# Kernel tuning notes

Hardware: AMD Instinct MI355X
Metric: run time of the kernel (lower is better)

## Reference

```python
import jax, jax.numpy as jnp
import numpy as np

N_CLUSTERS = 8
ENC_IN = 862
SEQ_LEN = 720
PRED_LEN = 336
BATCH = 64


def setup_inputs() -> dict:
    key = jax.random.key(0)
    k1, k2, k3, k4 = jax.random.split(key, 4)
    x = jax.random.normal(k1, (BATCH, ENC_IN, SEQ_LEN), dtype=jnp.float32)
    clusters = jax.random.randint(k2, (ENC_IN,), 0, N_CLUSTERS, dtype=jnp.int64)
    # Per-cluster Linear(seq_len -> pred_len): weight [P, S], bias [P], like nn.Linear
    bound = 1.0 / np.sqrt(SEQ_LEN)
    W = jax.random.uniform(k3, (N_CLUSTERS, PRED_LEN, SEQ_LEN), dtype=jnp.float32, minval=-bound, maxval=bound)
    b = jax.random.uniform(k4, (N_CLUSTERS, PRED_LEN), dtype=jnp.float32, minval=-bound, maxval=bound)
    return {"x": x, "clusters": clusters, "W": W, "b": b}


def reference(x, clusters, W, b):
    # Gather each channel's cluster weight/bias, then batched per-channel GEMV.
    Wc = W[clusters]            # [C, P, S]
    bc = b[clusters]            # [C, P]
    # out[b, c, p] = sum_s x[b, c, s] * Wc[c, p, s] + bc[c, p]
    out = jnp.einsum('bcs,cps->bcp', x, Wc) + bc[None, :, :]
    return out
```

## Files before the change

kernel.cpp:

```cpp
#include <hip/hip_runtime.h>
#include <stdint.h>

#define N_CL    8
#define C_IN    862
#define SEQ     720
#define SEQP    768
#define PRED    336
#define BATCH   64
#define BK      64
#define NCH     (SEQP / BK)
#define XBSTRIDE ((size_t)C_IN * SEQ)

typedef __attribute__((ext_vector_type(8))) __bf16 bf16x8;
typedef __attribute__((ext_vector_type(4))) float  floatx4;

__device__ __forceinline__ void async16(const void* g, void* l) {
  __builtin_amdgcn_global_load_lds(
      (__attribute__((address_space(1))) unsigned int*)(uintptr_t)g,
      (__attribute__((address_space(3))) unsigned int*)l,
      16, 0, 0);
}

__global__ void wconv_kernel(const float* __restrict__ W, __bf16* __restrict__ Wb) {
  const int row = blockIdx.x;
  const float* src = W + (size_t)row * SEQ;
  __bf16* dst = Wb + (size_t)row * SEQP;
  for (int s = threadIdx.x; s < SEQP; s += blockDim.x) {
    float v = (s < SEQ) ? src[s] : 0.0f;
    dst[s] = (__bf16)v;
  }
}

#define A_BYTES 8192
#define B_BYTES 43008

__global__ __launch_bounds__(256, 3) void clin_kernel(
    const float* __restrict__ x, const int* __restrict__ clusters,
    const __bf16* __restrict__ Wb, const float* __restrict__ bias,
    float* __restrict__ out) {
  __shared__ __attribute__((aligned(128))) unsigned char smem[A_BYTES + B_BYTES];
  unsigned char* As = smem;
  unsigned char* Bs = smem + A_BYTES;

  const int c    = blockIdx.x;
  const int cl   = clusters[c];
  const int tid  = threadIdx.x;
  const int wave = tid >> 6;
  const int lane = tid & 63;
  const int q    = lane >> 4;
  const int ln   = lane & 15;
  const int m7   = ln & 7;

  const float*  xc = x  + (size_t)c * SEQ;
  const __bf16* wc = Wb + (size_t)cl * PRED * SEQP;

  floatx4 acc[4][5];
  floatx4 accx[4];
#pragma unroll
  for (int mt = 0; mt < 4; ++mt) {
#pragma unroll
    for (int t = 0; t < 5; ++t) acc[mt][t] = (floatx4){0.f, 0.f, 0.f, 0.f};
    accx[mt] = (floatx4){0.f, 0.f, 0.f, 0.f};
  }

  const int ar  = tid >> 2;
  const int ag0 = (tid & 3) << 1;
  const int am  = ar & 7;
  const uint32_t aoff0 = (uint32_t)ar * 128 + (((ag0    ) ^ am) << 4);
  const uint32_t aoff1 = (uint32_t)ar * 128 + (((ag0 + 1) ^ am) << 4);
  const float* asrc = xc + (size_t)ar * XBSTRIDE;

  const int bB_r  = lane >> 3;
  const int bB_pg = lane & 7;

  const int nb = wave * 5;

  for (int chunk = 0; chunk < NCH; ++chunk) {
    const int k0 = chunk * BK;

    for (int i = wave; i < 42; i += 4) {
      int r  = (i << 3) + bB_r;
      int lg = bB_pg ^ (r & 7);
      async16(wc + (size_t)r * SEQP + k0 + (lg << 3), Bs + i * 1024);
    }

    if (k0 + BK <= SEQ) {
      const float* s = asrc + k0 + (ag0 << 3);
      floatx4 f0 = *(const floatx4*)(s);
      floatx4 f1 = *(const floatx4*)(s + 4);
      floatx4 f2 = *(const floatx4*)(s + 8);
      floatx4 f3 = *(const floatx4*)(s + 12);
      bf16x8 h0, h1;
      h0[0] = (__bf16)f0[0]; h0[1] = (__bf16)f0[1];
      h0[2] = (__bf16)f0[2]; h0[3] = (__bf16)f0[3];
      h0[4] = (__bf16)f1[0]; h0[5] = (__bf16)f1[1];
      h0[6] = (__bf16)f1[2]; h0[7] = (__bf16)f1[3];
      h1[0] = (__bf16)f2[0]; h1[1] = (__bf16)f2[1];
      h1[2] = (__bf16)f2[2]; h1[3] = (__bf16)f2[3];
      h1[4] = (__bf16)f3[0]; h1[5] = (__bf16)f3[1];
      h1[6] = (__bf16)f3[2]; h1[7] = (__bf16)f3[3];
      *(bf16x8*)(As + aoff0) = h0;
      *(bf16x8*)(As + aoff1) = h1;
    } else {
      float tmp[16];
#pragma unroll
      for (int j = 0; j < 16; ++j) {
        int k = k0 + (ag0 << 3) + j;
        tmp[j] = (k < SEQ) ? asrc[k] : 0.0f;
      }
      bf16x8 h0, h1;
#pragma unroll
      for (int j = 0; j < 8; ++j) { h0[j] = (__bf16)tmp[j]; h1[j] = (__bf16)tmp[8 + j]; }
      *(bf16x8*)(As + aoff0) = h0;
      *(bf16x8*)(As + aoff1) = h1;
    }
    __syncthreads();

#pragma unroll
    for (int kk = 0; kk < BK; kk += 32) {
      const int gA = (kk >> 3) + q;
      bf16x8 a[4];
#pragma unroll
      for (int mt = 0; mt < 4; ++mt)
        a[mt] = *(const bf16x8*)(As + ((mt << 4) + ln) * 128 + ((gA ^ m7) << 4));
#pragma unroll
      for (int t = 0; t < 5; ++t) {
        int n = ((nb + t) << 4) + ln;
        bf16x8 b = *(const bf16x8*)(Bs + n * 128 + ((gA ^ m7) << 4));
#pragma unroll
        for (int mt = 0; mt < 4; ++mt)
          acc[mt][t] = __builtin_amdgcn_mfma_f32_16x16x32_bf16(a[mt], b, acc[mt][t], 0, 0, 0);
      }
      if (wave == 3) {
        int n = (20 << 4) + ln;
        bf16x8 b = *(const bf16x8*)(Bs + n * 128 + ((gA ^ m7) << 4));
#pragma unroll
        for (int mt = 0; mt < 4; ++mt)
          accx[mt] = __builtin_amdgcn_mfma_f32_16x16x32_bf16(a[mt], b, accx[mt], 0, 0, 0);
      }
    }
    __syncthreads();
  }

  const float* bc = bias + cl * PRED;
#pragma unroll
  for (int t = 0; t < 5; ++t) {
    int p = ((nb + t) << 4) + ln;
    float bv = bc[p];
#pragma unroll
    for (int mt = 0; mt < 4; ++mt) {
#pragma unroll
      for (int r = 0; r < 4; ++r) {
        int brow = (mt << 4) + (q << 2) + r;
        out[((size_t)brow * C_IN + c) * PRED + p] = acc[mt][t][r] + bv;
      }
    }
  }
  if (wave == 3) {
    int p = (20 << 4) + ln;
    float bv = bc[p];
#pragma unroll
    for (int mt = 0; mt < 4; ++mt) {
#pragma unroll
      for (int r = 0; r < 4; ++r) {
        int brow = (mt << 4) + (q << 2) + r;
        out[((size_t)brow * C_IN + c) * PRED + p] = accx[mt][r] + bv;
      }
    }
  }
}

extern "C" void kernel_launch(void* const* d_in, const int* in_sizes, int n_in,
                              void* d_out, int out_size, void* d_ws, size_t ws_size,
                              hipStream_t stream) {
  const float* x   = (const float*)d_in[0];
  const int*   cls = (const int*)d_in[1];
  const float* W   = (const float*)d_in[2];
  const float* b   = (const float*)d_in[3];
  float* out = (float*)d_out;
  __bf16* Wb = (__bf16*)d_ws;

  hipLaunchKernelGGL(wconv_kernel, dim3(N_CL * PRED), dim3(256), 0, stream, W, Wb);
  hipLaunchKernelGGL(clin_kernel, dim3(C_IN), dim3(256), 0, stream,
                     x, cls, Wb, b, out);
}
```

Before: 307.8 us.

## Split channel GEMV across two blocks and double-buffer LDS chunks

Each channel is now handled by two blocks, each taking half of the prediction rows (176 and 160), which doubles the grid and balances tiles across waves. The K loop is double-buffered: the next chunk's weight async loads and x global loads are issued before the MFMA work on the current chunk, and there is one barrier per iteration instead of two. This aims to overlap memory latency with compute and to spread work over more CUs. In exchange each block uses more LDS and occupancy is lowered to 2 blocks per CU, and each x tile is now read and converted twice.

```diff
diff --git a/kernel.cpp b/kernel.cpp
--- a/kernel.cpp
+++ b/kernel.cpp
@@ -6,10 +6,15 @@
 #define SEQ     720
 #define SEQP    768
 #define PRED    336
-#define BATCH   64
 #define BK      64
-#define NCH     (SEQP / BK)
+#define NCH     12
 #define XBSTRIDE ((size_t)C_IN * SEQ)
+
+#define H0_ROWS 176
+#define H1_ROWS 160
+#define A_BYTES 8192
+#define B_BYTES (H0_ROWS * 128)
+#define BUF_BYTES (A_BYTES + B_BYTES)
 
 typedef __attribute__((ext_vector_type(8))) __bf16 bf16x8;
 typedef __attribute__((ext_vector_type(4))) float  floatx4;
@@ -31,18 +36,19 @@
   }
 }
 
-#define A_BYTES 8192
-#define B_BYTES 43008
-
-__global__ __launch_bounds__(256, 3) void clin_kernel(
+__global__ __launch_bounds__(256, 2) void clin_kernel(
     const float* __restrict__ x, const int* __restrict__ clusters,
     const __bf16* __restrict__ Wb, const float* __restrict__ bias,
     float* __restrict__ out) {
-  __shared__ __attribute__((aligned(128))) unsigned char smem[A_BYTES + B_BYTES];
-  unsigned char* As = smem;
-  unsigned char* Bs = smem + A_BYTES;
-
-  const int c    = blockIdx.x;
+  __shared__ __attribute__((aligned(128))) unsigned char smem[2 * BUF_BYTES];
+
+  const int bid  = blockIdx.x;
+  const int c    = bid >> 1;
+  const int half = bid & 1;
+  const int nrows = half ? H1_ROWS : H0_ROWS;
+  const int ntl   = half ? 10 : 11;
+  const int prow0 = half * H0_ROWS;
+
   const int cl   = clusters[c];
   const int tid  = threadIdx.x;
   const int wave = tid >> 6;
@@ -52,16 +58,13 @@
   const int m7   = ln & 7;
 
   const float*  xc = x  + (size_t)c * SEQ;
-  const __bf16* wc = Wb + (size_t)cl * PRED * SEQP;
-
-  floatx4 acc[4][5];
-  floatx4 accx[4];
-#pragma unroll
-  for (int mt = 0; mt < 4; ++mt) {
-#pragma unroll
-    for (int t = 0; t < 5; ++t) acc[mt][t] = (floatx4){0.f, 0.f, 0.f, 0.f};
-    accx[mt] = (floatx4){0.f, 0.f, 0.f, 0.f};
-  }
+  const __bf16* wc = Wb + (size_t)cl * PRED * SEQP + (size_t)prow0 * SEQP;
+
+  floatx4 acc[4][3];
+#pragma unroll
+  for (int mt = 0; mt < 4; ++mt)
+#pragma unroll
+    for (int t = 0; t < 3; ++t) acc[mt][t] = (floatx4){0.f, 0.f, 0.f, 0.f};
 
   const int ar  = tid >> 2;
   const int ag0 = (tid & 3) << 1;
@@ -72,49 +75,67 @@
 
   const int bB_r  = lane >> 3;
   const int bB_pg = lane & 7;
-
-  const int nb = wave * 5;
-
-  for (int chunk = 0; chunk < NCH; ++chunk) {
-    const int k0 = chunk * BK;
-
-    for (int i = wave; i < 42; i += 4) {
+  const int nBi   = nrows >> 3;
+
+  {
+    unsigned char* As = smem;
+    unsigned char* Bs = smem + A_BYTES;
+    for (int i = wave; i < nBi; i += 4) {
       int r  = (i << 3) + bB_r;
       int lg = bB_pg ^ (r & 7);
-      async16(wc + (size_t)r * SEQP + k0 + (lg << 3), Bs + i * 1024);
-    }
-
-    if (k0 + BK <= SEQ) {
-      const float* s = asrc + k0 + (ag0 << 3);
-      floatx4 f0 = *(const floatx4*)(s);
-      floatx4 f1 = *(const floatx4*)(s + 4);
-      floatx4 f2 = *(const floatx4*)(s + 8);
-      floatx4 f3 = *(const floatx4*)(s + 12);
-      bf16x8 h0, h1;
-      h0[0] = (__bf16)f0[0]; h0[1] = (__bf16)f0[1];
-      h0[2] = (__bf16)f0[2]; h0[3] = (__bf16)f0[3];
-      h0[4] = (__bf16)f1[0]; h0[5] = (__bf16)f1[1];
-      h0[6] = (__bf16)f1[2]; h0[7] = (__bf16)f1[3];
-      h1[0] = (__bf16)f2[0]; h1[1] = (__bf16)f2[1];
-      h1[2] = (__bf16)f2[2]; h1[3] = (__bf16)f2[3];
-      h1[4] = (__bf16)f3[0]; h1[5] = (__bf16)f3[1];
-      h1[6] = (__bf16)f3[2]; h1[7] = (__bf16)f3[3];
-      *(bf16x8*)(As + aoff0) = h0;
-      *(bf16x8*)(As + aoff1) = h1;
-    } else {
-      float tmp[16];
-#pragma unroll
-      for (int j = 0; j < 16; ++j) {
-        int k = k0 + (ag0 << 3) + j;
-        tmp[j] = (k < SEQ) ? asrc[k] : 0.0f;
-      }
-      bf16x8 h0, h1;
-#pragma unroll
-      for (int j = 0; j < 8; ++j) { h0[j] = (__bf16)tmp[j]; h1[j] = (__bf16)tmp[8 + j]; }
-      *(bf16x8*)(As + aoff0) = h0;
-      *(bf16x8*)(As + aoff1) = h1;
-    }
+      async16(wc + (size_t)r * SEQP + (lg << 3), Bs + i * 1024);
+    }
+    const float* s = asrc + (ag0 << 3);
+    floatx4 f0 = *(const floatx4*)(s);
+    floatx4 f1 = *(const floatx4*)(s + 4);
+    floatx4 f2 = *(const floatx4*)(s + 8);
+    floatx4 f3 = *(const floatx4*)(s + 12);
+    bf16x8 h0, h1;
+#pragma unroll
+    for (int j = 0; j < 4; ++j) {
+      h0[j]   = (__bf16)f0[j]; h0[4+j] = (__bf16)f1[j];
+      h1[j]   = (__bf16)f2[j]; h1[4+j] = (__bf16)f3[j];
+    }
+    *(bf16x8*)(As + aoff0) = h0;
+    *(bf16x8*)(As + aoff1) = h1;
+  }
+
+  for (int k = 0; k < NCH; ++k) {
     __syncthreads();
+    unsigned char* As  = smem + (k & 1) * BUF_BYTES;
+    unsigned char* Bs  = As + A_BYTES;
+    unsigned char* Asn = smem + ((k + 1) & 1) * BUF_BYTES;
+    unsigned char* Bsn = Asn + A_BYTES;
+
+    floatx4 f0, f1, f2, f3;
+    bool have_next = (k + 1 < NCH);
+    if (have_next) {
+      const int k0n = (k + 1) * BK;
+      if (k0n + BK <= SEQ) {
+        const float* s = asrc + k0n + (ag0 << 3);
+        f0 = *(const floatx4*)(s);
+        f1 = *(const floatx4*)(s + 4);
+        f2 = *(const floatx4*)(s + 8);
+        f3 = *(const floatx4*)(s + 12);
+      } else {
+        float tmp[16];
+#pragma unroll
+        for (int j = 0; j < 16; ++j) {
+          int kk2 = k0n + (ag0 << 3) + j;
+          tmp[j] = (kk2 < SEQ) ? asrc[kk2] : 0.0f;
+        }
+        f0 = (floatx4){tmp[0], tmp[1], tmp[2], tmp[3]};
+        f1 = (floatx4){tmp[4], tmp[5], tmp[6], tmp[7]};
+        f2 = (floatx4){tmp[8], tmp[9], tmp[10], tmp[11]};
+        f3 = (floatx4){tmp[12], tmp[13], tmp[14], tmp[15]};
+      }
+      const int k0b = (k + 1) * BK;
+      for (int i = wave; i < nBi; i += 4) {
+        int r  = (i << 3) + bB_r;
+        int lg = bB_pg ^ (r & 7);
+        async16(wc + (size_t)r * SEQP + k0b + (lg << 3), Bsn + i * 1024);
+      }
+    }
 
 #pragma unroll
     for (int kk = 0; kk < BK; kk += 32) {
@@ -124,47 +145,44 @@
       for (int mt = 0; mt < 4; ++mt)
         a[mt] = *(const bf16x8*)(As + ((mt << 4) + ln) * 128 + ((gA ^ m7) << 4));
 #pragma unroll
-      for (int t = 0; t < 5; ++t) {
-        int n = ((nb + t) << 4) + ln;
-        bf16x8 b = *(const bf16x8*)(Bs + n * 128 + ((gA ^ m7) << 4));
-#pragma unroll
-        for (int mt = 0; mt < 4; ++mt)
-          acc[mt][t] = __builtin_amdgcn_mfma_f32_16x16x32_bf16(a[mt], b, acc[mt][t], 0, 0, 0);
-      }
-      if (wave == 3) {
-        int n = (20 << 4) + ln;
-        bf16x8 b = *(const bf16x8*)(Bs + n * 128 + ((gA ^ m7) << 4));
-#pragma unroll
-        for (int mt = 0; mt < 4; ++mt)
-          accx[mt] = __builtin_amdgcn_mfma_f32_16x16x32_bf16(a[mt], b, accx[mt], 0, 0, 0);
-      }
-    }
-    __syncthreads();
-  }
-
-  const float* bc = bias + cl * PRED;
-#pragma unroll
-  for (int t = 0; t < 5; ++t) {
-    int p = ((nb + t) << 4) + ln;
-    float bv = bc[p];
-#pragma unroll
-    for (int mt = 0; mt < 4; ++mt) {
-#pragma unroll
-      for (int r = 0; r < 4; ++r) {
-        int brow = (mt << 4) + (q << 2) + r;
-        out[((size_t)brow * C_IN + c) * PRED + p] = acc[mt][t][r] + bv;
-      }
-    }
-  }
-  if (wave == 3) {
-    int p = (20 << 4) + ln;
-    float bv = bc[p];
-#pragma unroll
-    for (int mt = 0; mt < 4; ++mt) {
-#pragma unroll
-      for (int r = 0; r < 4; ++r) {
-        int brow = (mt << 4) + (q << 2) + r;
-        out[((size_t)brow * C_IN + c) * PRED + p] = accx[mt][r] + bv;
+      for (int t = 0; t < 3; ++t) {
+        int tl = wave + (t << 2);
+        if (tl < ntl) {
+          bf16x8 b = *(const bf16x8*)(Bs + ((tl << 4) + ln) * 128 + ((gA ^ m7) << 4));
+#pragma unroll
+          for (int mt = 0; mt < 4; ++mt)
+            acc[mt][t] = __builtin_amdgcn_mfma_f32_16x16x32_bf16(a[mt], b, acc[mt][t], 0, 0, 0);
+        }
+      }
+    }
+
+    if (have_next) {
+      bf16x8 h0, h1;
+#pragma unroll
+      for (int j = 0; j < 4; ++j) {
+        h0[j]   = (__bf16)f0[j]; h0[4+j] = (__bf16)f1[j];
+        h1[j]   = (__bf16)f2[j]; h1[4+j] = (__bf16)f3[j];
+      }
+      *(bf16x8*)(Asn + aoff0) = h0;
+      *(bf16x8*)(Asn + aoff1) = h1;
+    }
+  }
+
+  const float* bc = bias + cl * PRED + prow0;
+#pragma unroll
+  for (int t = 0; t < 3; ++t) {
+    int tl = wave + (t << 2);
+    if (tl < ntl) {
+      int p  = (tl << 4) + ln;
+      float bv = bc[p];
+      int pg = prow0 + p;
+#pragma unroll
+      for (int mt = 0; mt < 4; ++mt) {
+#pragma unroll
+        for (int r = 0; r < 4; ++r) {
+          int brow = (mt << 4) + (q << 2) + r;
+          out[((size_t)brow * C_IN + c) * PRED + pg] = acc[mt][t][r] + bv;
+        }
       }
     }
   }
@@ -181,6 +199,6 @@
   __bf16* Wb = (__bf16*)d_ws;
 
   hipLaunchKernelGGL(wconv_kernel, dim3(N_CL * PRED), dim3(256), 0, stream, W, Wb);
-  hipLaunchKernelGGL(clin_kernel, dim3(C_IN), dim3(256), 0, stream,
+  hipLaunchKernelGGL(clin_kernel, dim3(C_IN * 2), dim3(256), 0, stream,
                      x, cls, Wb, b, out);
 }
```

New measurement: 302.3 us. Within noise of the previous version (-1.8%).
